# Kernel optimization log

Hardware: AMD Instinct MI355X
Metric: run time of the kernel (lower is better)

Reference implementation:

```python
import jax, jax.numpy as jnp
import numpy as np

SINK = 4          # sink_size: tokens never evicted
MAX_CACHE = 8192  # sink_size + window_size
H = 32            # n_heads
HD = 128          # head_dim
D = H * HD        # d_model


def setup_inputs() -> dict:
    key = jax.random.key(0)
    ks = jax.random.split(key, 7)
    x = jax.random.normal(ks[0], (1, 1, D), dtype=jnp.float32)
    cached_k = jax.random.normal(ks[1], (1, H, MAX_CACHE, HD), dtype=jnp.float32)
    cached_v = jax.random.normal(ks[2], (1, H, MAX_CACHE, HD), dtype=jnp.float32)
    scale = 0.02
    Wq = jax.random.normal(ks[3], (D, D), dtype=jnp.float32) * scale
    Wk = jax.random.normal(ks[4], (D, D), dtype=jnp.float32) * scale
    Wv = jax.random.normal(ks[5], (D, D), dtype=jnp.float32) * scale
    Wo = jax.random.normal(ks[6], (D, D), dtype=jnp.float32) * scale
    return {"x": x, "cached_k": cached_k, "cached_v": cached_v,
            "Wq": Wq, "Wk": Wk, "Wv": Wv, "Wo": Wo}


def reference(x, cached_k, cached_v, Wq, Wk, Wv, Wo):
    """One StreamingLLM decode step with a full sink+window KV cache.

    x:        (1, 1, D)   single new token
    cached_k: (1, H, T, HD) with T == MAX_CACHE (cache at capacity)
    Returns (out, new_cached_k, new_cached_v) where out is (1, 1, D) and the
    new caches reflect sink-preserving eviction: [sink | recent[1:] | new].
    """
    B, S, _ = x.shape  # S == 1
    # projections for the new token -> (B, H, S, HD)
    q = (x @ Wq).reshape(B, S, H, HD).transpose(0, 2, 1, 3)
    k_new = (x @ Wk).reshape(B, S, H, HD).transpose(0, 2, 1, 3)
    v_new = (x @ Wv).reshape(B, S, H, HD).transpose(0, 2, 1, 3)

    # attend over past cache + new token (causal: single query sees everything)
    keys = jnp.concatenate([cached_k, k_new], axis=2)   # (B, H, T+1, HD)
    vals = jnp.concatenate([cached_v, v_new], axis=2)
    inv_sqrt_d = np.float32(1.0 / np.sqrt(HD))
    scores = jnp.einsum('bhqd,bhkd->bhqk', q, keys) * inv_sqrt_d
    attn = jax.nn.softmax(scores, axis=-1)
    ctx = jnp.einsum('bhqk,bhkd->bhqd', attn, vals)     # (B, H, 1, HD)
    out = ctx.transpose(0, 2, 1, 3).reshape(B, S, H * HD) @ Wo

    # KVCache.update full-cache branch: keep sink, drop oldest recent, append new
    new_cached_k = jnp.concatenate(
        [cached_k[:, :, :SINK], cached_k[:, :, SINK + 1:], k_new], axis=2)
    new_cached_v = jnp.concatenate(
        [cached_v[:, :, :SINK], cached_v[:, :, SINK + 1:], v_new], axis=2)
    return out, new_cached_k, new_cached_v
```

## Files before the change

kernel.cpp:

```cpp
#include <hip/hip_runtime.h>

#define D     4096
#define NH    32
#define HD    128
#define TT    8192
#define SINKN 4
#define NC    64
#define CS    128
#define ICH   64
#define PBSTR (HD + 2)

__global__ __launch_bounds__(256) void qkv_partial(
        const float* __restrict__ x,
        const float* __restrict__ Wq,
        const float* __restrict__ Wk,
        const float* __restrict__ Wv,
        float* __restrict__ partA,
        float* __restrict__ out) {
    int bid = blockIdx.x;
    int tid = threadIdx.x;
    if (bid < 16) out[bid * 256 + tid] = 0.f;
    int mat = bid >> 8;
    int rem = bid & 255;
    int jb  = rem >> 6;
    int ic  = rem & 63;
    const float* Wm = (mat == 0) ? Wq : (mat == 1) ? Wk : Wv;
    int j0 = jb * 1024 + tid * 4;
    int i0 = ic * 64;
    __shared__ float xs[64];
    if (tid < 64) xs[tid] = x[i0 + tid];
    __syncthreads();
    float4 acc = {0.f, 0.f, 0.f, 0.f};
    const float* Wp = Wm + (size_t)i0 * D + j0;
    #pragma unroll 16
    for (int i = 0; i < 64; ++i) {
        float4 w = *(const float4*)Wp;
        float xv = xs[i];
        acc.x += xv * w.x; acc.y += xv * w.y;
        acc.z += xv * w.z; acc.w += xv * w.w;
        Wp += D;
    }
    *(float4*)(partA + (size_t)(mat * ICH + ic) * D + j0) = acc;
}

__global__ __launch_bounds__(256) void attn_chunk(
        const float* __restrict__ partA,
        const float* __restrict__ K,
        const float* __restrict__ V,
        float* __restrict__ newK,
        float* __restrict__ newV,
        float* __restrict__ partB) {
    int bid = blockIdx.x;
    int h = bid >> 6;
    int c = bid & 63;
    int t0 = c * CS;
    int tid  = threadIdx.x;
    int wave = tid >> 6;
    int lane = tid & 63;
    int l31  = lane & 31;
    int half = lane >> 5;

    __shared__ float qs[HD];
    __shared__ float sc[CS];
    __shared__ float ml[2];
    __shared__ float ctx8[8][HD];

    {
        int d  = tid & 127;
        int hh = tid >> 7;
        const float* p = partA + (size_t)(hh * 32) * D + (size_t)h * HD + d;
        float s = 0.f;
        #pragma unroll
        for (int i = 0; i < 32; ++i) s += p[(size_t)i * D];
        ctx8[hh][d] = s;
    }
    __syncthreads();
    if (tid < HD) qs[tid] = ctx8[0][tid] + ctx8[1][tid];
    __syncthreads();

    float4 qv = *(const float4*)(qs + 4 * l31);
    const float scale = 0.08838834764831845f;

    const float* Kh = K    + (size_t)h * TT * HD;
    float*      nKh = newK + (size_t)h * TT * HD;
    for (int kk = 0; kk < 16; ++kk) {
        int r = t0 + kk * 8 + wave * 2 + half;
        float4 kv = *(const float4*)(Kh + (size_t)r * HD + 4 * l31);
        float p = qv.x * kv.x + qv.y * kv.y + qv.z * kv.z + qv.w * kv.w;
        p += __shfl_xor(p, 16, 64);
        p += __shfl_xor(p, 8, 64);
        p += __shfl_xor(p, 4, 64);
        p += __shfl_xor(p, 2, 64);
        p += __shfl_xor(p, 1, 64);
        if (l31 == 0) sc[r - t0] = p * scale;
        if (r != SINKN) {
            int dst = (r < SINKN) ? r : r - 1;
            *(float4*)(nKh + (size_t)dst * HD + 4 * l31) = kv;
        }
    }
    __syncthreads();
    if (wave == 0) {
        float s0 = sc[lane], s1 = sc[lane + 64];
        float m = fmaxf(s0, s1);
        #pragma unroll
        for (int off = 32; off; off >>= 1) m = fmaxf(m, __shfl_xor(m, off, 64));
        float w0 = __expf(s0 - m), w1 = __expf(s1 - m);
        sc[lane] = w0; sc[lane + 64] = w1;
        float l = w0 + w1;
        #pragma unroll
        for (int off = 32; off; off >>= 1) l += __shfl_xor(l, off, 64);
        if (lane == 0) { ml[0] = m; ml[1] = l; }
    }
    __syncthreads();
    const float* Vh = V    + (size_t)h * TT * HD;
    float*      nVh = newV + (size_t)h * TT * HD;
    float a0 = 0.f, a1 = 0.f, a2 = 0.f, a3 = 0.f;
    for (int kk = 0; kk < 16; ++kk) {
        int r = t0 + kk * 8 + wave * 2 + half;
        float4 vv = *(const float4*)(Vh + (size_t)r * HD + 4 * l31);
        float w = sc[r - t0];
        a0 += w * vv.x; a1 += w * vv.y; a2 += w * vv.z; a3 += w * vv.w;
        if (r != SINKN) {
            int dst = (r < SINKN) ? r : r - 1;
            *(float4*)(nVh + (size_t)dst * HD + 4 * l31) = vv;
        }
    }
    int g = wave * 2 + half;
    ctx8[g][4 * l31 + 0] = a0;
    ctx8[g][4 * l31 + 1] = a1;
    ctx8[g][4 * l31 + 2] = a2;
    ctx8[g][4 * l31 + 3] = a3;
    __syncthreads();
    float* pbE = partB + ((size_t)h * (NC + 1) + c) * PBSTR;
    if (tid < HD) {
        float s = 0.f;
        #pragma unroll
        for (int gg = 0; gg < 8; ++gg) s += ctx8[gg][tid];
        pbE[2 + tid] = s;
    }
    if (tid == 0) { pbE[0] = ml[0]; pbE[1] = ml[1]; }

    if (c == 0) {
        float kd = 0.f, vd = 0.f;
        if (tid < HD) {
            const float* pk = partA + (size_t)(ICH) * D + (size_t)h * HD + tid;
            const float* pv = partA + (size_t)(2 * ICH) * D + (size_t)h * HD + tid;
            #pragma unroll
            for (int i = 0; i < ICH; ++i) {
                kd += pk[(size_t)i * D];
                vd += pv[(size_t)i * D];
            }
            newK[((size_t)h * TT + (TT - 1)) * HD + tid] = kd;
            newV[((size_t)h * TT + (TT - 1)) * HD + tid] = vd;
        }
        __syncthreads();
        if (tid < HD) ctx8[0][tid] = qs[tid] * kd;
        __syncthreads();
        float* pbN = partB + ((size_t)h * (NC + 1) + NC) * PBSTR;
        if (tid < 64) {
            float s = ctx8[0][tid] + ctx8[0][tid + 64];
            #pragma unroll
            for (int off = 32; off; off >>= 1) s += __shfl_xor(s, off, 64);
            if (tid == 0) { pbN[0] = s * scale; pbN[1] = 1.0f; }
        }
        if (tid < HD) pbN[2 + tid] = vd;
    }
}

__global__ __launch_bounds__(128) void out_fused(
        const float* __restrict__ partB,
        const float* __restrict__ Wo,
        float* __restrict__ out) {
    int bid = blockIdx.x;
    int jb = bid >> 6;
    int ic = bid & 63;
    int tid = threadIdx.x;
    int h  = ic >> 1;
    int d0 = (ic & 1) * 64;

    __shared__ float marr[NC + 1], larr[NC + 1], wgt[NC + 1];
    __shared__ float ctx[64];
    __shared__ float Ls;

    const float* pb = partB + (size_t)h * (NC + 1) * PBSTR;
    if (tid <= NC) {
        marr[tid] = pb[tid * PBSTR];
        larr[tid] = pb[tid * PBSTR + 1];
    }
    __syncthreads();
    float M = marr[0];
    #pragma unroll
    for (int cc = 1; cc <= NC; ++cc) M = fmaxf(M, marr[cc]);
    if (tid <= NC) wgt[tid] = __expf(marr[tid] - M);
    __syncthreads();
    if (tid < 64) {
        float s = wgt[tid] * larr[tid] + ((tid == 0) ? wgt[NC] * larr[NC] : 0.f);
        #pragma unroll
        for (int off = 32; off; off >>= 1) s += __shfl_xor(s, off, 64);
        if (tid == 0) Ls = s;
    }
    __syncthreads();
    if (tid < 64) {
        const float* pc = pb + 2 + d0 + tid;
        float acc = 0.f;
        #pragma unroll
        for (int cc = 0; cc <= NC; ++cc) acc += wgt[cc] * pc[cc * PBSTR];
        ctx[tid] = acc / Ls;
    }
    __syncthreads();

    int j0 = jb * 512 + tid * 4;
    float4 acc = {0.f, 0.f, 0.f, 0.f};
    const float* Wp = Wo + (size_t)(ic * 64) * D + j0;
    #pragma unroll 16
    for (int i = 0; i < 64; ++i) {
        float4 w = *(const float4*)Wp;
        float xv = ctx[i];
        acc.x += xv * w.x; acc.y += xv * w.y;
        acc.z += xv * w.z; acc.w += xv * w.w;
        Wp += D;
    }
    atomicAdd(&out[j0 + 0], acc.x);
    atomicAdd(&out[j0 + 1], acc.y);
    atomicAdd(&out[j0 + 2], acc.z);
    atomicAdd(&out[j0 + 3], acc.w);
}

extern "C" void kernel_launch(void* const* d_in, const int* in_sizes, int n_in,
                              void* d_out, int out_size, void* d_ws, size_t ws_size,
                              hipStream_t stream) {
    const float* x  = (const float*)d_in[0];
    const float* cK = (const float*)d_in[1];
    const float* cV = (const float*)d_in[2];
    const float* Wq = (const float*)d_in[3];
    const float* Wk = (const float*)d_in[4];
    const float* Wv = (const float*)d_in[5];
    const float* Wo = (const float*)d_in[6];

    float* out  = (float*)d_out;
    float* newK = out + D;
    float* newV = newK + (size_t)NH * TT * HD;

    float* ws    = (float*)d_ws;
    float* partA = ws;
    float* partB = partA + 3 * ICH * D;

    qkv_partial<<<768,     256, 0, stream>>>(x, Wq, Wk, Wv, partA, out);
    attn_chunk <<<NH * NC, 256, 0, stream>>>(partA, cK, cV, newK, newV, partB);
    out_fused  <<<512,     128, 0, stream>>>(partB, Wo, out);
}
```

Before: 182.4 us.

## Overlap K/V projections with cached attention and fold new-token term into combine

The Q projection now runs alone in the first kernel. The K and V GEMVs move into the attention kernel as extra blocks, so their weight streaming runs concurrently with the cache attention and copy work. The new token's score and value are computed in the output kernel, which also writes the appended K/V row. This removes the serial dependency of attention on the K/V projections, at the cost of every output block redundantly reducing the 64 q/k/v partial chunks. The attention loops are also unrolled, with the copy stores moved ahead of the reductions.

```diff
diff --git a/kernel.cpp b/kernel.cpp
--- a/kernel.cpp
+++ b/kernel.cpp
@@ -10,28 +10,23 @@
 #define ICH   64
 #define PBSTR (HD + 2)
 
-__global__ __launch_bounds__(256) void qkv_partial(
+__global__ __launch_bounds__(256) void q_gemv(
         const float* __restrict__ x,
         const float* __restrict__ Wq,
-        const float* __restrict__ Wk,
-        const float* __restrict__ Wv,
-        float* __restrict__ partA,
+        float* __restrict__ partQ,
         float* __restrict__ out) {
     int bid = blockIdx.x;
     int tid = threadIdx.x;
     if (bid < 16) out[bid * 256 + tid] = 0.f;
-    int mat = bid >> 8;
-    int rem = bid & 255;
-    int jb  = rem >> 6;
-    int ic  = rem & 63;
-    const float* Wm = (mat == 0) ? Wq : (mat == 1) ? Wk : Wv;
+    int jb = bid >> 6;
+    int ic = bid & 63;
     int j0 = jb * 1024 + tid * 4;
     int i0 = ic * 64;
     __shared__ float xs[64];
     if (tid < 64) xs[tid] = x[i0 + tid];
     __syncthreads();
     float4 acc = {0.f, 0.f, 0.f, 0.f};
-    const float* Wp = Wm + (size_t)i0 * D + j0;
+    const float* Wp = Wq + (size_t)i0 * D + j0;
     #pragma unroll 16
     for (int i = 0; i < 64; ++i) {
         float4 w = *(const float4*)Wp;
@@ -40,35 +35,66 @@
         acc.z += xv * w.z; acc.w += xv * w.w;
         Wp += D;
     }
-    *(float4*)(partA + (size_t)(mat * ICH + ic) * D + j0) = acc;
-}
-
-__global__ __launch_bounds__(256) void attn_chunk(
-        const float* __restrict__ partA,
+    *(float4*)(partQ + (size_t)ic * D + j0) = acc;
+}
+
+__global__ __launch_bounds__(256) void attn_kv(
+        const float* __restrict__ x,
+        const float* __restrict__ partQ,
+        const float* __restrict__ Wk,
+        const float* __restrict__ Wv,
         const float* __restrict__ K,
         const float* __restrict__ V,
         float* __restrict__ newK,
         float* __restrict__ newV,
+        float* __restrict__ partKV,
         float* __restrict__ partB) {
     int bid = blockIdx.x;
-    int h = bid >> 6;
-    int c = bid & 63;
+    int tid = threadIdx.x;
+
+    __shared__ float xs[64];
+    __shared__ float qs[HD];
+    __shared__ float sc[CS];
+    __shared__ float ml[2];
+    __shared__ float ctx8[8][HD];
+
+    if (bid < 512) {
+        int mat = bid >> 8;
+        int rem = bid & 255;
+        int jb  = rem >> 6;
+        int ic  = rem & 63;
+        const float* Wm = mat ? Wv : Wk;
+        int j0 = jb * 1024 + tid * 4;
+        int i0 = ic * 64;
+        if (tid < 64) xs[tid] = x[i0 + tid];
+        __syncthreads();
+        float4 acc = {0.f, 0.f, 0.f, 0.f};
+        const float* Wp = Wm + (size_t)i0 * D + j0;
+        #pragma unroll 16
+        for (int i = 0; i < 64; ++i) {
+            float4 w = *(const float4*)Wp;
+            float xv = xs[i];
+            acc.x += xv * w.x; acc.y += xv * w.y;
+            acc.z += xv * w.z; acc.w += xv * w.w;
+            Wp += D;
+        }
+        *(float4*)(partKV + (size_t)(mat * ICH + ic) * D + j0) = acc;
+        return;
+    }
+
+    int b = bid - 512;
+    int h = b >> 6;
+    int c = b & 63;
     int t0 = c * CS;
-    int tid  = threadIdx.x;
     int wave = tid >> 6;
     int lane = tid & 63;
     int l31  = lane & 31;
     int half = lane >> 5;
 
-    __shared__ float qs[HD];
-    __shared__ float sc[CS];
-    __shared__ float ml[2];
-    __shared__ float ctx8[8][HD];
-
     {
         int d  = tid & 127;
         int hh = tid >> 7;
-        const float* p = partA + (size_t)(hh * 32) * D + (size_t)h * HD + d;
+        const float* p = partQ + (size_t)(hh * 32) * D + (size_t)h * HD + d;
         float s = 0.f;
         #pragma unroll
         for (int i = 0; i < 32; ++i) s += p[(size_t)i * D];
@@ -83,9 +109,14 @@
 
     const float* Kh = K    + (size_t)h * TT * HD;
     float*      nKh = newK + (size_t)h * TT * HD;
+    #pragma unroll 4
     for (int kk = 0; kk < 16; ++kk) {
         int r = t0 + kk * 8 + wave * 2 + half;
         float4 kv = *(const float4*)(Kh + (size_t)r * HD + 4 * l31);
+        if (r != SINKN) {
+            int dst = (r < SINKN) ? r : r - 1;
+            *(float4*)(nKh + (size_t)dst * HD + 4 * l31) = kv;
+        }
         float p = qv.x * kv.x + qv.y * kv.y + qv.z * kv.z + qv.w * kv.w;
         p += __shfl_xor(p, 16, 64);
         p += __shfl_xor(p, 8, 64);
@@ -93,10 +124,6 @@
         p += __shfl_xor(p, 2, 64);
         p += __shfl_xor(p, 1, 64);
         if (l31 == 0) sc[r - t0] = p * scale;
-        if (r != SINKN) {
-            int dst = (r < SINKN) ? r : r - 1;
-            *(float4*)(nKh + (size_t)dst * HD + 4 * l31) = kv;
-        }
     }
     __syncthreads();
     if (wave == 0) {
@@ -115,15 +142,16 @@
     const float* Vh = V    + (size_t)h * TT * HD;
     float*      nVh = newV + (size_t)h * TT * HD;
     float a0 = 0.f, a1 = 0.f, a2 = 0.f, a3 = 0.f;
+    #pragma unroll 4
     for (int kk = 0; kk < 16; ++kk) {
         int r = t0 + kk * 8 + wave * 2 + half;
         float4 vv = *(const float4*)(Vh + (size_t)r * HD + 4 * l31);
-        float w = sc[r - t0];
-        a0 += w * vv.x; a1 += w * vv.y; a2 += w * vv.z; a3 += w * vv.w;
         if (r != SINKN) {
             int dst = (r < SINKN) ? r : r - 1;
             *(float4*)(nVh + (size_t)dst * HD + 4 * l31) = vv;
         }
+        float w = sc[r - t0];
+        a0 += w * vv.x; a1 += w * vv.y; a2 += w * vv.z; a3 += w * vv.w;
     }
     int g = wave * 2 + half;
     ctx8[g][4 * l31 + 0] = a0;
@@ -131,7 +159,7 @@
     ctx8[g][4 * l31 + 2] = a2;
     ctx8[g][4 * l31 + 3] = a3;
     __syncthreads();
-    float* pbE = partB + ((size_t)h * (NC + 1) + c) * PBSTR;
+    float* pbE = partB + ((size_t)h * NC + c) * PBSTR;
     if (tid < HD) {
         float s = 0.f;
         #pragma unroll
@@ -139,37 +167,15 @@
         pbE[2 + tid] = s;
     }
     if (tid == 0) { pbE[0] = ml[0]; pbE[1] = ml[1]; }
-
-    if (c == 0) {
-        float kd = 0.f, vd = 0.f;
-        if (tid < HD) {
-            const float* pk = partA + (size_t)(ICH) * D + (size_t)h * HD + tid;
-            const float* pv = partA + (size_t)(2 * ICH) * D + (size_t)h * HD + tid;
-            #pragma unroll
-            for (int i = 0; i < ICH; ++i) {
-                kd += pk[(size_t)i * D];
-                vd += pv[(size_t)i * D];
-            }
-            newK[((size_t)h * TT + (TT - 1)) * HD + tid] = kd;
-            newV[((size_t)h * TT + (TT - 1)) * HD + tid] = vd;
-        }
-        __syncthreads();
-        if (tid < HD) ctx8[0][tid] = qs[tid] * kd;
-        __syncthreads();
-        float* pbN = partB + ((size_t)h * (NC + 1) + NC) * PBSTR;
-        if (tid < 64) {
-            float s = ctx8[0][tid] + ctx8[0][tid + 64];
-            #pragma unroll
-            for (int off = 32; off; off >>= 1) s += __shfl_xor(s, off, 64);
-            if (tid == 0) { pbN[0] = s * scale; pbN[1] = 1.0f; }
-        }
-        if (tid < HD) pbN[2 + tid] = vd;
-    }
 }
 
 __global__ __launch_bounds__(128) void out_fused(
+        const float* __restrict__ partQ,
+        const float* __restrict__ partKV,
         const float* __restrict__ partB,
         const float* __restrict__ Wo,
+        float* __restrict__ newK,
+        float* __restrict__ newV,
         float* __restrict__ out) {
     int bid = blockIdx.x;
     int jb = bid >> 6;
@@ -178,23 +184,50 @@
     int h  = ic >> 1;
     int d0 = (ic & 1) * 64;
 
-    __shared__ float marr[NC + 1], larr[NC + 1], wgt[NC + 1];
-    __shared__ float ctx[64];
+    const float* pq = partQ  + (size_t)h * HD + tid;
+    const float* pk = partKV + (size_t)h * HD + tid;
+    const float* pv = partKV + (size_t)ICH * D + (size_t)h * HD + tid;
+    float qd = 0.f, kd = 0.f, vd = 0.f;
+    #pragma unroll
+    for (int i = 0; i < ICH; ++i) {
+        qd += pq[(size_t)i * D];
+        kd += pk[(size_t)i * D];
+        vd += pv[(size_t)i * D];
+    }
+    if (jb == 0 && (ic & 1) == 0) {
+        newK[((size_t)h * TT + (TT - 1)) * HD + tid] = kd;
+        newV[((size_t)h * TT + (TT - 1)) * HD + tid] = vd;
+    }
+
+    __shared__ float red[HD];
+    __shared__ float vsh[HD];
+    __shared__ float marr[NC], larr[NC], wgt[NC + 1];
+    __shared__ float ctxs[64];
     __shared__ float Ls;
 
-    const float* pb = partB + (size_t)h * (NC + 1) * PBSTR;
-    if (tid <= NC) {
+    vsh[tid] = vd;
+    red[tid] = qd * kd;
+    __syncthreads();
+    for (int s = 64; s > 0; s >>= 1) {
+        if (tid < s) red[tid] += red[tid + s];
+        __syncthreads();
+    }
+    float s_new = red[0] * 0.08838834764831845f;
+
+    const float* pb = partB + (size_t)h * NC * PBSTR;
+    if (tid < NC) {
         marr[tid] = pb[tid * PBSTR];
         larr[tid] = pb[tid * PBSTR + 1];
     }
     __syncthreads();
-    float M = marr[0];
+    float M = s_new;
     #pragma unroll
-    for (int cc = 1; cc <= NC; ++cc) M = fmaxf(M, marr[cc]);
-    if (tid <= NC) wgt[tid] = __expf(marr[tid] - M);
+    for (int cc = 0; cc < NC; ++cc) M = fmaxf(M, marr[cc]);
+    if (tid < NC) wgt[tid] = __expf(marr[tid] - M);
+    else if (tid == NC) wgt[NC] = __expf(s_new - M);
     __syncthreads();
     if (tid < 64) {
-        float s = wgt[tid] * larr[tid] + ((tid == 0) ? wgt[NC] * larr[NC] : 0.f);
+        float s = wgt[tid] * larr[tid] + ((tid == 0) ? wgt[NC] : 0.f);
         #pragma unroll
         for (int off = 32; off; off >>= 1) s += __shfl_xor(s, off, 64);
         if (tid == 0) Ls = s;
@@ -202,10 +235,10 @@
     __syncthreads();
     if (tid < 64) {
         const float* pc = pb + 2 + d0 + tid;
-        float acc = 0.f;
-        #pragma unroll
-        for (int cc = 0; cc <= NC; ++cc) acc += wgt[cc] * pc[cc * PBSTR];
-        ctx[tid] = acc / Ls;
+        float acc = wgt[NC] * vsh[d0 + tid];
+        #pragma unroll
+        for (int cc = 0; cc < NC; ++cc) acc += wgt[cc] * pc[cc * PBSTR];
+        ctxs[tid] = acc / Ls;
     }
     __syncthreads();
 
@@ -215,7 +248,7 @@
     #pragma unroll 16
     for (int i = 0; i < 64; ++i) {
         float4 w = *(const float4*)Wp;
-        float xv = ctx[i];
+        float xv = ctxs[i];
         acc.x += xv * w.x; acc.y += xv * w.y;
         acc.z += xv * w.z; acc.w += xv * w.w;
         Wp += D;
@@ -241,11 +274,14 @@
     float* newK = out + D;
     float* newV = newK + (size_t)NH * TT * HD;
 
-    float* ws    = (float*)d_ws;
-    float* partA = ws;
-    float* partB = partA + 3 * ICH * D;
-
-    qkv_partial<<<768,     256, 0, stream>>>(x, Wq, Wk, Wv, partA, out);
-    attn_chunk <<<NH * NC, 256, 0, stream>>>(partA, cK, cV, newK, newV, partB);
-    out_fused  <<<512,     128, 0, stream>>>(partB, Wo, out);
-}
+    float* ws     = (float*)d_ws;
+    float* partQ  = ws;
+    float* partKV = partQ + (size_t)ICH * D;
+    float* partB  = partKV + (size_t)2 * ICH * D;
+
+    q_gemv   <<<256,        256, 0, stream>>>(x, Wq, partQ, out);
+    attn_kv  <<<512 + NH*NC,256, 0, stream>>>(x, partQ, Wk, Wv, cK, cV,
+                                              newK, newV, partKV, partB);
+    out_fused<<<512,        128, 0, stream>>>(partQ, partKV, partB, Wo,
+                                              newK, newV, out);
+}
```

After: 221.8 us. 1.22x slower.
